# Kernel optimization log

Measured on AMD Instinct MI355X. Metric: run time of the kernel, lower is better.

The kernel has to match this reference:

```python
import jax, jax.numpy as jnp
import numpy as np

OFFSETS = (1, 2, 4, 8, 16, 64, 96, 192, 384, 512, 768, 1024)
J = 12
J_LARGE = 8  # offsets with index >= 4 use phase rotation


def _shift(x, d):
    """Return x shifted so out[..., n, :] = x[..., n-d, :]; zeros where n < d.
    Shift is along axis 2 (the sequence axis of [B,H,N,...])."""
    pad = [(0, 0)] * x.ndim
    pad[2] = (d, 0)
    return jnp.pad(x, pad)[:, :, : x.shape[2]]


def setup_inputs() -> dict:
    key = jax.random.key(0)
    ks = jax.random.split(key, 9)
    B, H, N, HD = 2, 16, 4096, 64
    f = jnp.float32
    q = jax.random.normal(ks[0], (B, H, N, HD), f)
    k = jax.random.normal(ks[1], (B, H, N, HD), f)
    v = jax.random.normal(ks[2], (B, H, N, HD), f)
    pb = jax.random.normal(ks[3], (J, H), f) * 0.1          # per-offset per-head score bias
    se = jax.random.normal(ks[4], (J, HD), f) * 0.1         # per-offset score embedding
    phase_base = jax.random.normal(ks[5], (J_LARGE, H, 2), f) * 0.1
    phase_gain = jax.random.normal(ks[6], (J_LARGE, H, 2), f) * 0.1
    y_pre = jax.random.normal(ks[7], (B, H, N, 2), f)       # query-side phase features
    z_pre = jax.random.normal(ks[8], (B, H, N, 2), f)       # key-side phase features
    return dict(q=q, k=k, v=v, pb=pb, se=se, phase_base=phase_base,
                phase_gain=phase_gain, y_pre=y_pre, z_pre=z_pre)


def reference(q, k, v, pb, se, phase_base, phase_gain, y_pre, z_pre):
    B, H, N, HD = q.shape
    sc = 1.0 / float(np.sqrt(HD))
    n_idx = jnp.arange(N)

    # --- scores over the J fixed causal offsets: s_i[n] = (q_n . (k_{n-d} + se_i)) * sc + pb[i,h]
    scores = []
    for i, d in enumerate(OFFSETS):
        ks_ = _shift(k, d)  # key at n - d
        s = (jnp.einsum('bhnd,bhnd->bhn', q, ks_)
             + jnp.einsum('bhnd,d->bhn', q, se[i])) * sc
        s = s + pb[i][None, :, None]
        valid = (n_idx >= d)[None, None, :]
        scores.append(jnp.where(valid, s, -jnp.inf))
    scores = jnp.stack(scores, axis=-1)  # [B,H,N,J]

    lse = jax.nn.logsumexp(scores, axis=-1)            # [B,H,N]
    safe_lse = jnp.where(jnp.isfinite(lse), lse, 0.0)  # rows with no valid offset -> alpha = 0
    alpha = jnp.exp(scores - safe_lse[..., None])      # [B,H,N,J]; -inf scores give exactly 0

    # --- weighted sum of (phase-rotated) values
    out = jnp.zeros_like(q)
    for i, d in enumerate(OFFSETS):
        vs = _shift(v, d)  # value at n - d: [B,H,N,HD]
        if i >= 4:
            pi = i - 4
            zs = _shift(z_pre, d)  # key-side phase features at n - d: [B,H,N,2]
            # theta_p = base[pi,h,p] + gain[pi,h,p] * y_pre[n,p] * z_pre[n-d,p]
            theta = (phase_base[pi][None, :, None, :]
                     + phase_gain[pi][None, :, None, :] * y_pre * zs)  # [B,H,N,2]
            c, s_ = jnp.cos(theta), jnp.sin(theta)
            v0, v1, v2, v3 = vs[..., 0], vs[..., 1], vs[..., 2], vs[..., 3]
            rot = jnp.stack([c[..., 0] * v0 - s_[..., 0] * v1,
                             s_[..., 0] * v0 + c[..., 0] * v1,
                             c[..., 1] * v2 - s_[..., 1] * v3,
                             s_[..., 1] * v2 + c[..., 1] * v3], axis=-1)
            vs = jnp.concatenate([rot, vs[..., 4:]], axis=-1)
        out = out + alpha[..., i:i + 1] * vs
    return out
```

## Files before the change

kernel.cpp:

```cpp
#include <hip/hip_runtime.h>


namespace {

constexpr int J   = 12;
constexpr int B_  = 2;
constexpr int H_  = 16;
constexpr int N_  = 4096;
constexpr int HD_ = 64;
constexpr int OFFS[J] = {1, 2, 4, 8, 16, 64, 96, 192, 384, 512, 768, 1024};

using f32x4 = __attribute__((ext_vector_type(4))) float;
using f32x2 = __attribute__((ext_vector_type(2))) float;

#define GLOAD4(dst, off, base)                                              \
    asm volatile("global_load_dwordx4 %0, %1, %2"                           \
                 : "=v"(dst) : "v"(off), "s"(base) : "memory")
#define GLOAD2(dst, off, base)                                              \
    asm volatile("global_load_dwordx2 %0, %1, %2"                           \
                 : "=v"(dst) : "v"(off), "s"(base) : "memory")

template <int CTRL>
__device__ __forceinline__ float dpp_add(float x) {
    int s = __builtin_amdgcn_update_dpp(0, __builtin_bit_cast(int, x),
                                        CTRL, 0xF, 0xF, false);
    return x + __builtin_bit_cast(float, s);
}

__global__ __launch_bounds__(256, 4) void dsqg_kernel(
    const float* __restrict__ q, const float* __restrict__ k,
    const float* __restrict__ v, const float* __restrict__ pb,
    const float* __restrict__ se, const float* __restrict__ phase_base,
    const float* __restrict__ phase_gain, const float* __restrict__ y_pre,
    const float* __restrict__ z_pre, float* __restrict__ out)
{
    __shared__ f32x4 seS[J * 16];
    __shared__ int   dtab[8];

    const int raw = blockIdx.x;
    const int per = gridDim.x >> 3;
    const int wid = (raw & 7) * per + (raw >> 3);

    const int bh    = wid >> 8;
    const int chunk = wid & 255;
    const int h     = bh & (H_ - 1);

    const int tid  = threadIdx.x;
    const int lane = tid & 63;
    const int wave = tid >> 6;
    const int grp  = lane & 15;
    const int n    = chunk * 16 + wave * 4 + (lane >> 4);

    if (tid < J * 16) seS[tid] = ((const f32x4*)se)[tid];
    if (tid < 8)      dtab[tid] = OFFS[tid + 4];

    const size_t bhbytes = (size_t)bh * (N_ * HD_ * 4);
    const char* qb  = (const char*)q + bhbytes;
    const char* kb  = (const char*)k + bhbytes;
    const char* vb  = (const char*)v + bhbytes;
    char*       ob  = (char*)out + bhbytes;
    const char* yb  = (const char*)y_pre + (size_t)bh * (N_ * 8);
    const char* zb  = (const char*)z_pre + (size_t)bh * (N_ * 8);
    const char* pbb = (const char*)phase_base;
    const char* pgb = (const char*)phase_gain;

    const uint32_t gb   = (uint32_t)grp << 4;
    const uint32_t rowb = ((uint32_t)n << 8) + gb;
    const uint32_t nb8  = (uint32_t)n << 3;

    bool ok[J];
    uint32_t offb[J];
#pragma unroll
    for (int i = 0; i < J; ++i) {
        ok[i]   = (n >= OFFS[i]);
        offb[i] = ok[i] ? (rowb - ((uint32_t)OFFS[i] << 8)) : gb;
    }

    __syncthreads();

    const int t8 = grp & 7;
    const int dl = dtab[t8];
    const bool okl = (n >= dl);
    const uint32_t zol  = okl ? (uint32_t)(n - dl) << 3 : 0u;
    const uint32_t vxol = okl ? (uint32_t)(n - dl) << 8 : 0u;
    const uint32_t pofs = (uint32_t)(t8 * H_ + h) << 3;

    f32x4 qr;
    GLOAD4(qr, rowb, qb);
    f32x4 kr[J];
#pragma unroll
    for (int i = 0; i < J; ++i) GLOAD4(kr[i], offb[i], kb);
    f32x2 yp;  GLOAD2(yp,  nb8,  yb);
    f32x2 zl;  GLOAD2(zl,  zol,  zb);
    f32x2 pbs; GLOAD2(pbs, pofs, pbb);
    f32x2 pgn; GLOAD2(pgn, pofs, pgb);

    asm volatile("s_waitcnt vmcnt(4)" ::: "memory");
    __builtin_amdgcn_sched_barrier(0);

    float p[J];
#pragma unroll
    for (int i = 0; i < J; ++i) {
        const f32x4 seg = seS[i * 16 + grp];
        float t = qr.x * (kr[i].x + seg.x);
        t = fmaf(qr.y, kr[i].y + seg.y, t);
        t = fmaf(qr.z, kr[i].z + seg.z, t);
        p[i] = fmaf(qr.w, kr[i].w + seg.w, t);
    }

    __builtin_amdgcn_sched_barrier(0);
    f32x4 vr[J];
#pragma unroll
    for (int i = 0; i < J; ++i) GLOAD4(vr[i], offb[i], vb);
    f32x4 vx;
    GLOAD4(vx, vxol, vb);
    __builtin_amdgcn_sched_barrier(0);

#pragma unroll
    for (int i = 0; i < J; ++i) {
        p[i] = dpp_add<0xB1>(p[i]);
        p[i] = dpp_add<0x4E>(p[i]);
        p[i] = dpp_add<0x124>(p[i]);
        p[i] = dpp_add<0x128>(p[i]);
    }

    const float sc = 0.125f;
    float e[J];
    float sum = 0.f;
#pragma unroll
    for (int i = 0; i < J; ++i) {
        const float si = fmaf(p[i], sc, pb[i * H_ + h]);
        e[i] = ok[i] ? __expf(si) : 0.f;
        sum += e[i];
    }

    asm volatile("s_waitcnt vmcnt(0)" ::: "memory");
    __builtin_amdgcn_sched_barrier(0);

    const float s01 = (t8 & 1) ? e[5]  : e[4];
    const float s23 = (t8 & 1) ? e[7]  : e[6];
    const float s45 = (t8 & 1) ? e[9]  : e[8];
    const float s67 = (t8 & 1) ? e[11] : e[10];
    const float sA  = (t8 & 2) ? s23 : s01;
    const float sB  = (t8 & 2) ? s67 : s45;
    const float esel = (t8 & 4) ? sB : sA;

    const float th0 = fmaf(pgn.x, yp.x * zl.x, pbs.x);
    const float th1 = fmaf(pgn.y, yp.y * zl.y, pbs.y);
    const float c0 = __cosf(th0), s0 = __sinf(th0);
    const float c1 = __cosf(th1), s1 = __sinf(th1);
    f32x4 cx;
    cx.x = esel * (c0 * vx.x - s0 * vx.y);
    cx.y = esel * (s0 * vx.x + c0 * vx.y);
    cx.z = esel * (c1 * vx.z - s1 * vx.w);
    cx.w = esel * (s1 * vx.z + c1 * vx.w);

#pragma unroll
    for (int st = 0; st < 1; ++st) { }
    cx.x = dpp_add<0xB1>(cx.x); cx.y = dpp_add<0xB1>(cx.y);
    cx.z = dpp_add<0xB1>(cx.z); cx.w = dpp_add<0xB1>(cx.w);
    cx.x = dpp_add<0x4E>(cx.x); cx.y = dpp_add<0x4E>(cx.y);
    cx.z = dpp_add<0x4E>(cx.z); cx.w = dpp_add<0x4E>(cx.w);
    cx.x = dpp_add<0x124>(cx.x); cx.y = dpp_add<0x124>(cx.y);
    cx.z = dpp_add<0x124>(cx.z); cx.w = dpp_add<0x124>(cx.w);

    float4 accl = make_float4(0.f, 0.f, 0.f, 0.f);
#pragma unroll
    for (int i = 0; i < 4; ++i) {
        accl.x = fmaf(e[i], vr[i].x, accl.x);
        accl.y = fmaf(e[i], vr[i].y, accl.y);
        accl.z = fmaf(e[i], vr[i].z, accl.z);
        accl.w = fmaf(e[i], vr[i].w, accl.w);
    }
    float4 acch = accl;
#pragma unroll
    for (int i = 4; i < J; ++i) {
        acch.x = fmaf(e[i], vr[i].x, acch.x);
        acch.y = fmaf(e[i], vr[i].y, acch.y);
        acch.z = fmaf(e[i], vr[i].z, acch.z);
        acch.w = fmaf(e[i], vr[i].w, acch.w);
    }
    const bool lo = (grp == 0);
    float4 acc;
    acc.x = lo ? accl.x + cx.x : acch.x;
    acc.y = lo ? accl.y + cx.y : acch.y;
    acc.z = lo ? accl.z + cx.z : acch.z;
    acc.w = lo ? accl.w + cx.w : acch.w;

    float4 res;
    if (n >= 1) {
        const float inv = __builtin_amdgcn_rcpf(sum);
        res = make_float4(acc.x * inv, acc.y * inv, acc.z * inv, acc.w * inv);
    } else {
        res = make_float4(0.f, 0.f, 0.f, 0.f);
    }
    *(float4*)(ob + rowb) = res;
}

}

extern "C" void kernel_launch(void* const* d_in, const int* in_sizes, int n_in,
                              void* d_out, int out_size, void* d_ws, size_t ws_size,
                              hipStream_t stream) {
    const float* q          = (const float*)d_in[0];
    const float* k          = (const float*)d_in[1];
    const float* v          = (const float*)d_in[2];
    const float* pb         = (const float*)d_in[3];
    const float* se         = (const float*)d_in[4];
    const float* phase_base = (const float*)d_in[5];
    const float* phase_gain = (const float*)d_in[6];
    const float* y_pre      = (const float*)d_in[7];
    const float* z_pre      = (const float*)d_in[8];
    float* out              = (float*)d_out;

    const int positions = B_ * H_ * N_;
    const int blocks    = positions / 16;
    dsqg_kernel<<<blocks, 256, 0, stream>>>(q, k, v, pb, se, phase_base,
                                            phase_gain, y_pre, z_pre, out);
}
```

Before: 183.7 us.

## Stage a shared K/V window in LDS for the five short offsets

```diff
diff --git a/kernel.cpp b/kernel.cpp
--- a/kernel.cpp
+++ b/kernel.cpp
@@ -9,6 +9,8 @@
 constexpr int N_  = 4096;
 constexpr int HD_ = 64;
 constexpr int OFFS[J] = {1, 2, 4, 8, 16, 64, 96, 192, 384, 512, 768, 1024};
+constexpr int T_  = 64;
+constexpr int W_  = 80;
 
 using f32x4 = __attribute__((ext_vector_type(4))) float;
 using f32x2 = __attribute__((ext_vector_type(2))) float;
@@ -27,174 +29,224 @@
     return x + __builtin_bit_cast(float, s);
 }
 
-__global__ __launch_bounds__(256, 4) void dsqg_kernel(
+__global__ __launch_bounds__(256, 3) void dsqg_kernel(
     const float* __restrict__ q, const float* __restrict__ k,
     const float* __restrict__ v, const float* __restrict__ pb,
     const float* __restrict__ se, const float* __restrict__ phase_base,
     const float* __restrict__ phase_gain, const float* __restrict__ y_pre,
     const float* __restrict__ z_pre, float* __restrict__ out)
 {
+    __shared__ f32x4 kS[W_ * 16];
+    __shared__ f32x4 vS[W_ * 16];
     __shared__ f32x4 seS[J * 16];
-    __shared__ int   dtab[8];
 
     const int raw = blockIdx.x;
     const int per = gridDim.x >> 3;
     const int wid = (raw & 7) * per + (raw >> 3);
 
-    const int bh    = wid >> 8;
-    const int chunk = wid & 255;
-    const int h     = bh & (H_ - 1);
+    const int bh  = wid >> 6;
+    const int blk = wid & 63;
+    const int h   = bh & (H_ - 1);
+    const int P   = blk * T_;
 
     const int tid  = threadIdx.x;
     const int lane = tid & 63;
     const int wave = tid >> 6;
     const int grp  = lane & 15;
-    const int n    = chunk * 16 + wave * 4 + (lane >> 4);
+    const int sub  = lane >> 4;
 
     if (tid < J * 16) seS[tid] = ((const f32x4*)se)[tid];
-    if (tid < 8)      dtab[tid] = OFFS[tid + 4];
 
     const size_t bhbytes = (size_t)bh * (N_ * HD_ * 4);
-    const char* qb  = (const char*)q + bhbytes;
-    const char* kb  = (const char*)k + bhbytes;
-    const char* vb  = (const char*)v + bhbytes;
-    char*       ob  = (char*)out + bhbytes;
-    const char* yb  = (const char*)y_pre + (size_t)bh * (N_ * 8);
-    const char* zb  = (const char*)z_pre + (size_t)bh * (N_ * 8);
-    const char* pbb = (const char*)phase_base;
-    const char* pgb = (const char*)phase_gain;
-
-    const uint32_t gb   = (uint32_t)grp << 4;
-    const uint32_t rowb = ((uint32_t)n << 8) + gb;
-    const uint32_t nb8  = (uint32_t)n << 3;
-
-    bool ok[J];
-    uint32_t offb[J];
-#pragma unroll
-    for (int i = 0; i < J; ++i) {
-        ok[i]   = (n >= OFFS[i]);
-        offb[i] = ok[i] ? (rowb - ((uint32_t)OFFS[i] << 8)) : gb;
+    const char* qb = (const char*)q + bhbytes;
+    const char* kb = (const char*)k + bhbytes;
+    const char* vb = (const char*)v + bhbytes;
+    char*       ob = (char*)out + bhbytes;
+    const char* yb = (const char*)y_pre + (size_t)bh * (N_ * 8);
+    const char* zb = (const char*)z_pre + (size_t)bh * (N_ * 8);
+
+    {
+        const int r0 = P - 16;
+#pragma unroll
+        for (int t = 0; t < (W_ * 16) / 256; ++t) {
+            const int idx = t * 256 + tid;
+            const int row = idx >> 4;
+            const int col = idx & 15;
+            int gr = r0 + row;
+            gr = gr < 0 ? 0 : gr;
+            const uint32_t go = ((uint32_t)gr << 8) + ((uint32_t)col << 4);
+            kS[idx] = *(const f32x4*)(kb + go);
+            vS[idx] = *(const f32x4*)(vb + go);
+        }
     }
 
+    const int t8  = grp & 7;
+    const int d01 = (t8 & 1) ? 64   : 16;
+    const int d23 = (t8 & 1) ? 192  : 96;
+    const int d45 = (t8 & 1) ? 512  : 384;
+    const int d67 = (t8 & 1) ? 1024 : 768;
+    const int dA  = (t8 & 2) ? d23 : d01;
+    const int dB  = (t8 & 2) ? d67 : d45;
+    const int dl  = (t8 & 4) ? dB : dA;
+
+    const uint32_t pofs = (uint32_t)(t8 * H_ + h) << 3;
+    const f32x2 pbs = *(const f32x2*)((const char*)phase_base + pofs);
+    const f32x2 pgn = *(const f32x2*)((const char*)phase_gain + pofs);
+    float pbh[J];
+#pragma unroll
+    for (int i = 0; i < J; ++i) pbh[i] = pb[i * H_ + h];
+
     __syncthreads();
 
-    const int t8 = grp & 7;
-    const int dl = dtab[t8];
-    const bool okl = (n >= dl);
-    const uint32_t zol  = okl ? (uint32_t)(n - dl) << 3 : 0u;
-    const uint32_t vxol = okl ? (uint32_t)(n - dl) << 8 : 0u;
-    const uint32_t pofs = (uint32_t)(t8 * H_ + h) << 3;
-
-    f32x4 qr;
-    GLOAD4(qr, rowb, qb);
-    f32x4 kr[J];
-#pragma unroll
-    for (int i = 0; i < J; ++i) GLOAD4(kr[i], offb[i], kb);
-    f32x2 yp;  GLOAD2(yp,  nb8,  yb);
-    f32x2 zl;  GLOAD2(zl,  zol,  zb);
-    f32x2 pbs; GLOAD2(pbs, pofs, pbb);
-    f32x2 pgn; GLOAD2(pgn, pofs, pgb);
-
-    asm volatile("s_waitcnt vmcnt(4)" ::: "memory");
-    __builtin_amdgcn_sched_barrier(0);
-
-    float p[J];
-#pragma unroll
-    for (int i = 0; i < J; ++i) {
-        const f32x4 seg = seS[i * 16 + grp];
-        float t = qr.x * (kr[i].x + seg.x);
-        t = fmaf(qr.y, kr[i].y + seg.y, t);
-        t = fmaf(qr.z, kr[i].z + seg.z, t);
-        p[i] = fmaf(qr.w, kr[i].w + seg.w, t);
+    const float sc = 0.125f;
+
+#pragma unroll
+    for (int j = 0; j < 4; ++j) {
+        const int n = P + wave * 16 + j * 4 + sub;
+        const uint32_t rowb = ((uint32_t)n << 8) + ((uint32_t)grp << 4);
+        const uint32_t nb8  = (uint32_t)n << 3;
+
+        bool ok[J];
+#pragma unroll
+        for (int i = 0; i < J; ++i) ok[i] = (n >= OFFS[i]);
+
+        uint32_t offb[7];
+#pragma unroll
+        for (int i = 5; i < J; ++i)
+            offb[i - 5] = ok[i] ? (rowb - ((uint32_t)OFFS[i] << 8))
+                                : ((uint32_t)grp << 4);
+
+        const bool okl = (n >= dl);
+        const uint32_t zol  = okl ? (uint32_t)(n - dl) << 3 : 0u;
+        const uint32_t vxol = okl ? (uint32_t)(n - dl) << 8 : 0u;
+
+        f32x4 qr;
+        GLOAD4(qr, rowb, qb);
+        f32x4 kr[7];
+#pragma unroll
+        for (int i = 0; i < 7; ++i) GLOAD4(kr[i], offb[i], kb);
+        f32x2 yp; GLOAD2(yp, nb8, yb);
+        f32x2 zl; GLOAD2(zl, zol, zb);
+
+        asm volatile("s_waitcnt vmcnt(2)" ::: "memory");
+        __builtin_amdgcn_sched_barrier(0);
+
+        float p[J];
+#pragma unroll
+        for (int i = 0; i < 5; ++i) {
+            const int rel = n - OFFS[i] - P + 16;
+            const f32x4 kk  = kS[rel * 16 + grp];
+            const f32x4 seg = seS[i * 16 + grp];
+            float t = qr.x * (kk.x + seg.x);
+            t = fmaf(qr.y, kk.y + seg.y, t);
+            t = fmaf(qr.z, kk.z + seg.z, t);
+            p[i] = fmaf(qr.w, kk.w + seg.w, t);
+        }
+#pragma unroll
+        for (int i = 5; i < J; ++i) {
+            const f32x4 kk  = kr[i - 5];
+            const f32x4 seg = seS[i * 16 + grp];
+            float t = qr.x * (kk.x + seg.x);
+            t = fmaf(qr.y, kk.y + seg.y, t);
+            t = fmaf(qr.z, kk.z + seg.z, t);
+            p[i] = fmaf(qr.w, kk.w + seg.w, t);
+        }
+
+        __builtin_amdgcn_sched_barrier(0);
+        f32x4 vr[7];
+#pragma unroll
+        for (int i = 0; i < 7; ++i) GLOAD4(vr[i], offb[i], vb);
+        f32x4 vx;
+        GLOAD4(vx, vxol, vb);
+        __builtin_amdgcn_sched_barrier(0);
+
+#pragma unroll
+        for (int i = 0; i < J; ++i) {
+            p[i] = dpp_add<0xB1>(p[i]);
+            p[i] = dpp_add<0x4E>(p[i]);
+            p[i] = dpp_add<0x124>(p[i]);
+            p[i] = dpp_add<0x128>(p[i]);
+        }
+
+        float e[J];
+        float sum = 0.f;
+#pragma unroll
+        for (int i = 0; i < J; ++i) {
+            const float si = fmaf(p[i], sc, pbh[i]);
+            e[i] = ok[i] ? __expf(si) : 0.f;
+            sum += e[i];
+        }
+
+        asm volatile("s_waitcnt vmcnt(0)" ::: "memory");
+        __builtin_amdgcn_sched_barrier(0);
+
+        const float s01 = (t8 & 1) ? e[5]  : e[4];
+        const float s23 = (t8 & 1) ? e[7]  : e[6];
+        const float s45 = (t8 & 1) ? e[9]  : e[8];
+        const float s67 = (t8 & 1) ? e[11] : e[10];
+        const float sA  = (t8 & 2) ? s23 : s01;
+        const float sB  = (t8 & 2) ? s67 : s45;
+        const float esel = (t8 & 4) ? sB : sA;
+
+        const float th0 = fmaf(pgn.x, yp.x * zl.x, pbs.x);
+        const float th1 = fmaf(pgn.y, yp.y * zl.y, pbs.y);
+        const float c0 = __cosf(th0), s0 = __sinf(th0);
+        const float c1 = __cosf(th1), s1 = __sinf(th1);
+        f32x4 cx;
+        cx.x = esel * (c0 * vx.x - s0 * vx.y);
+        cx.y = esel * (s0 * vx.x + c0 * vx.y);
+        cx.z = esel * (c1 * vx.z - s1 * vx.w);
+        cx.w = esel * (s1 * vx.z + c1 * vx.w);
+
+        cx.x = dpp_add<0xB1>(cx.x);  cx.y = dpp_add<0xB1>(cx.y);
+        cx.z = dpp_add<0xB1>(cx.z);  cx.w = dpp_add<0xB1>(cx.w);
+        cx.x = dpp_add<0x4E>(cx.x);  cx.y = dpp_add<0x4E>(cx.y);
+        cx.z = dpp_add<0x4E>(cx.z);  cx.w = dpp_add<0x4E>(cx.w);
+        cx.x = dpp_add<0x124>(cx.x); cx.y = dpp_add<0x124>(cx.y);
+        cx.z = dpp_add<0x124>(cx.z); cx.w = dpp_add<0x124>(cx.w);
+
+        float4 accl = make_float4(0.f, 0.f, 0.f, 0.f);
+#pragma unroll
+        for (int i = 0; i < 4; ++i) {
+            const int rel = n - OFFS[i] - P + 16;
+            const f32x4 vv = vS[rel * 16 + grp];
+            accl.x = fmaf(e[i], vv.x, accl.x);
+            accl.y = fmaf(e[i], vv.y, accl.y);
+            accl.z = fmaf(e[i], vv.z, accl.z);
+            accl.w = fmaf(e[i], vv.w, accl.w);
+        }
+        float4 acch = accl;
+        {
+            const int rel = n - 16 - P + 16;
+            const f32x4 vv = vS[rel * 16 + grp];
+            acch.x = fmaf(e[4], vv.x, acch.x);
+            acch.y = fmaf(e[4], vv.y, acch.y);
+            acch.z = fmaf(e[4], vv.z, acch.z);
+            acch.w = fmaf(e[4], vv.w, acch.w);
+        }
+#pragma unroll
+        for (int i = 5; i < J; ++i) {
+            acch.x = fmaf(e[i], vr[i - 5].x, acch.x);
+            acch.y = fmaf(e[i], vr[i - 5].y, acch.y);
+            acch.z = fmaf(e[i], vr[i - 5].z, acch.z);
+            acch.w = fmaf(e[i], vr[i - 5].w, acch.w);
+        }
+        const bool lo = (grp == 0);
+        float4 acc;
+        acc.x = lo ? accl.x + cx.x : acch.x;
+        acc.y = lo ? accl.y + cx.y : acch.y;
+        acc.z = lo ? accl.z + cx.z : acch.z;
+        acc.w = lo ? accl.w + cx.w : acch.w;
+
+        float4 res;
+        if (n >= 1) {
+            const float inv = __builtin_amdgcn_rcpf(sum);
+            res = make_float4(acc.x * inv, acc.y * inv, acc.z * inv, acc.w * inv);
+        } else {
+            res = make_float4(0.f, 0.f, 0.f, 0.f);
+        }
+        *(float4*)(ob + rowb) = res;
     }
-
-    __builtin_amdgcn_sched_barrier(0);
-    f32x4 vr[J];
-#pragma unroll
-    for (int i = 0; i < J; ++i) GLOAD4(vr[i], offb[i], vb);
-    f32x4 vx;
-    GLOAD4(vx, vxol, vb);
-    __builtin_amdgcn_sched_barrier(0);
-
-#pragma unroll
-    for (int i = 0; i < J; ++i) {
-        p[i] = dpp_add<0xB1>(p[i]);
-        p[i] = dpp_add<0x4E>(p[i]);
-        p[i] = dpp_add<0x124>(p[i]);
-        p[i] = dpp_add<0x128>(p[i]);
-    }
-
-    const float sc = 0.125f;
-    float e[J];
-    float sum = 0.f;
-#pragma unroll
-    for (int i = 0; i < J; ++i) {
-        const float si = fmaf(p[i], sc, pb[i * H_ + h]);
-        e[i] = ok[i] ? __expf(si) : 0.f;
-        sum += e[i];
-    }
-
-    asm volatile("s_waitcnt vmcnt(0)" ::: "memory");
-    __builtin_amdgcn_sched_barrier(0);
-
-    const float s01 = (t8 & 1) ? e[5]  : e[4];
-    const float s23 = (t8 & 1) ? e[7]  : e[6];
-    const float s45 = (t8 & 1) ? e[9]  : e[8];
-    const float s67 = (t8 & 1) ? e[11] : e[10];
-    const float sA  = (t8 & 2) ? s23 : s01;
-    const float sB  = (t8 & 2) ? s67 : s45;
-    const float esel = (t8 & 4) ? sB : sA;
-
-    const float th0 = fmaf(pgn.x, yp.x * zl.x, pbs.x);
-    const float th1 = fmaf(pgn.y, yp.y * zl.y, pbs.y);
-    const float c0 = __cosf(th0), s0 = __sinf(th0);
-    const float c1 = __cosf(th1), s1 = __sinf(th1);
-    f32x4 cx;
-    cx.x = esel * (c0 * vx.x - s0 * vx.y);
-    cx.y = esel * (s0 * vx.x + c0 * vx.y);
-    cx.z = esel * (c1 * vx.z - s1 * vx.w);
-    cx.w = esel * (s1 * vx.z + c1 * vx.w);
-
-#pragma unroll
-    for (int st = 0; st < 1; ++st) { }
-    cx.x = dpp_add<0xB1>(cx.x); cx.y = dpp_add<0xB1>(cx.y);
-    cx.z = dpp_add<0xB1>(cx.z); cx.w = dpp_add<0xB1>(cx.w);
-    cx.x = dpp_add<0x4E>(cx.x); cx.y = dpp_add<0x4E>(cx.y);
-    cx.z = dpp_add<0x4E>(cx.z); cx.w = dpp_add<0x4E>(cx.w);
-    cx.x = dpp_add<0x124>(cx.x); cx.y = dpp_add<0x124>(cx.y);
-    cx.z = dpp_add<0x124>(cx.z); cx.w = dpp_add<0x124>(cx.w);
-
-    float4 accl = make_float4(0.f, 0.f, 0.f, 0.f);
-#pragma unroll
-    for (int i = 0; i < 4; ++i) {
-        accl.x = fmaf(e[i], vr[i].x, accl.x);
-        accl.y = fmaf(e[i], vr[i].y, accl.y);
-        accl.z = fmaf(e[i], vr[i].z, accl.z);
-        accl.w = fmaf(e[i], vr[i].w, accl.w);
-    }
-    float4 acch = accl;
-#pragma unroll
-    for (int i = 4; i < J; ++i) {
-        acch.x = fmaf(e[i], vr[i].x, acch.x);
-        acch.y = fmaf(e[i], vr[i].y, acch.y);
-        acch.z = fmaf(e[i], vr[i].z, acch.z);
-        acch.w = fmaf(e[i], vr[i].w, acch.w);
-    }
-    const bool lo = (grp == 0);
-    float4 acc;
-    acc.x = lo ? accl.x + cx.x : acch.x;
-    acc.y = lo ? accl.y + cx.y : acch.y;
-    acc.z = lo ? accl.z + cx.z : acch.z;
-    acc.w = lo ? accl.w + cx.w : acch.w;
-
-    float4 res;
-    if (n >= 1) {
-        const float inv = __builtin_amdgcn_rcpf(sum);
-        res = make_float4(acc.x * inv, acc.y * inv, acc.z * inv, acc.w * inv);
-    } else {
-        res = make_float4(0.f, 0.f, 0.f, 0.f);
-    }
-    *(float4*)(ob + rowb) = res;
 }
 
 }
@@ -214,7 +266,7 @@
     float* out              = (float*)d_out;
 
     const int positions = B_ * H_ * N_;
-    const int blocks    = positions / 16;
+    const int blocks    = positions / T_;
     dsqg_kernel<<<blocks, 256, 0, stream>>>(q, k, v, pb, se, phase_base,
                                             phase_gain, y_pre, z_pre, out);
 }
```

Result: faster. 172.2 us (-6.2%).
